# Performance work log

Measured on AMD Instinct MI355X. Metric: run time of the kernel, lower is better.

Reference implementation:

```python
import jax, jax.numpy as jnp
import numpy as np

# Model dims
B, N, D_MODEL, N_HEADS = 8, 4096, 512, 8
EXPAND = 2
D1 = (EXPAND * D_MODEL) // N_HEADS * N_HEADS      # 1024
HEAD_DIM = D1 // N_HEADS                          # 128
RANK, NK = 32, 16
GAMMA = 0.999


def setup_inputs() -> dict:
    key = jax.random.key(0)
    ks = jax.random.split(key, 24)

    def p(i, shape, std=0.02):
        return std * jax.random.normal(ks[i], shape, dtype=jnp.float32)

    def toep_params(i0):
        # SKI low-rank Toeplitz operator params: kernel values at NK inducing
        # lag positions, factorized as (h, nk, r) @ (h, r, d), plus lag-0 term.
        return (p(i0, (N_HEADS, 1, HEAD_DIM), 1.0),        # zero lag
                p(i0 + 1, (N_HEADS, NK, RANK), 0.1),       # pos lags A
                p(i0 + 2, (N_HEADS, RANK, HEAD_DIM), 0.1), # pos lags B
                p(i0 + 3, (N_HEADS, NK, RANK), 0.1),       # neg lags A
                p(i0 + 4, (N_HEADS, RANK, HEAD_DIM), 0.1)) # neg lags B

    t1 = toep_params(7)
    t2 = toep_params(12)
    return {
        'x': jax.random.normal(ks[0], (B, N, D_MODEL), dtype=jnp.float32),
        'u_w': p(1, (D1, D_MODEL)), 'u_b': p(2, (D1,)),
        'v_w': p(3, (D1, D_MODEL)), 'v_b': p(4, (D1,)),
        'o_w': p(5, (D_MODEL, D1)), 'o_b': p(6, (D_MODEL,)),
        't1_zero': t1[0], 't1_pa': t1[1], 't1_pb': t1[2], 't1_na': t1[3], 't1_nb': t1[4],
        't2_zero': t2[0], 't2_pa': t2[1], 't2_pb': t2[2], 't2_na': t2[3], 't2_nb': t2[4],
    }


def _build_kernel(zero, pos_a, pos_b, neg_a, neg_b, n):
    """Build circular-conv kernel a of shape (h, 2n, d): a[k]=t(k), a[2n-k]=t(-k)."""
    h, nk, _ = pos_a.shape
    d = pos_b.shape[-1]
    tm_pos = jnp.einsum('hkr,hrd->hkd', pos_a, pos_b)   # kernel at inducing lags
    tm_neg = jnp.einsum('hkr,hrd->hkd', neg_a, neg_b)
    lags = jnp.arange(1, n, dtype=jnp.float32)          # lags 1..n-1
    # linear interpolation from NK inducing points to n-1 lags
    pos_f = (lags - 1.0) / max(n - 2, 1) * (nk - 1)
    lo = jnp.floor(pos_f).astype(jnp.int32)
    hi = jnp.minimum(lo + 1, nk - 1)
    w = (pos_f - lo)[None, :, None]
    decay = (GAMMA ** lags)[None, :, None]              # exponential decay bias
    t_pos = ((1.0 - w) * tm_pos[:, lo] + w * tm_pos[:, hi]) * decay
    t_neg = ((1.0 - w) * tm_neg[:, lo] + w * tm_neg[:, hi]) * decay
    return jnp.concatenate(
        [zero, t_pos, jnp.zeros((h, 1, d), t_pos.dtype), jnp.flip(t_neg, axis=1)],
        axis=1)


def _toep_apply(x, zero, pos_a, pos_b, neg_a, neg_b):
    # x: (b, n, g) with g = h*d; multi-head Toeplitz mixing along axis 1 via FFT.
    b, n, g = x.shape
    h = zero.shape[0]
    d = g // h
    xh = x.reshape(b, n, h, d).transpose(0, 2, 1, 3)    # (b, h, n, d)
    a = _build_kernel(zero, pos_a, pos_b, neg_a, neg_b, n)  # (h, 2n, d)
    y = jnp.fft.irfft(
        jnp.fft.rfft(xh, 2 * n, axis=2) * jnp.fft.rfft(a, axis=1)[None],
        2 * n, axis=2)[:, :, :n]
    return y.transpose(0, 2, 1, 3).reshape(b, n, g)


def reference(x, u_w, u_b, v_w, v_b, o_w, o_b,
              t1_zero, t1_pa, t1_pb, t1_na, t1_nb,
              t2_zero, t2_pa, t2_pb, t2_na, t2_nb):
    b, n, _ = x.shape
    H = int(np.sqrt(n))
    W = n // H
    u = jax.nn.silu(x @ u_w.T + u_b)
    v = jax.nn.silu(x @ v_w.T + v_b)
    g = v.shape[-1]
    t1 = (t1_zero, t1_pa, t1_pb, t1_na, t1_nb)
    t2 = (t2_zero, t2_pa, t2_pb, t2_na, t2_nb)
    # path 1: mix along W (rows) with toep1, then along H (cols) with toep2
    o1 = _toep_apply(v.reshape(b * H, W, g), *t1)
    o1 = o1.reshape(b, H, W, g).transpose(0, 2, 1, 3).reshape(b * W, H, g)
    o1 = _toep_apply(o1, *t2)
    o1 = o1.reshape(b, W, H, g).transpose(0, 2, 1, 3).reshape(b, H * W, g)
    # path 2: mix along H with toep2, then along W with toep1
    v2 = v.reshape(b, H, W, g).transpose(0, 2, 1, 3).reshape(b * W, H, g)
    o2 = _toep_apply(v2, *t2)
    o2 = o2.reshape(b, W, H, g).transpose(0, 2, 1, 3).reshape(b * H, W, g)
    o2 = _toep_apply(o2, *t1)
    o2 = o2.reshape(b, H * W, g)
    # SiLU gate + output projection
    return (u * (o1 + o2)) @ o_w.T + o_b
```

## Files before the change

kernel.cpp:

```cpp
#include <hip/hip_runtime.h>
#include <hip/hip_bf16.h>
#include <hip/hip_fp16.h>

typedef __bf16 bf16;
typedef bf16 bf16x2 __attribute__((ext_vector_type(2)));
typedef bf16 bf16x4 __attribute__((ext_vector_type(4)));
typedef bf16 bf16x8 __attribute__((ext_vector_type(8)));
typedef float f32x2 __attribute__((ext_vector_type(2)));
typedef float f32x4 __attribute__((ext_vector_type(4)));

__device__ __forceinline__ void gload_lds16(const void* g, void* l) {
  __builtin_amdgcn_global_load_lds((__attribute__((address_space(1))) void*)g,
                                   (__attribute__((address_space(3))) void*)l,
                                   16, 0, 0);
}

__device__ __forceinline__ f32x2 fma2(f32x2 a, f32x2 b, f32x2 c) {
  return __builtin_elementwise_fma(a, b, c);
}


__global__ void cast_f32_to_bf16(const float* __restrict__ in, bf16* __restrict__ out, int n4) {
  int i = blockIdx.x * blockDim.x + threadIdx.x;
  if (i >= n4) return;
  float4 v = ((const float4*)in)[i];
  bf16x4 o = {(bf16)v.x, (bf16)v.y, (bf16)v.z, (bf16)v.w};
  ((bf16x4*)out)[i] = o;
}

__global__ void cast_w3(const float* __restrict__ uw, const float* __restrict__ vw,
                        const float* __restrict__ ow,
                        bf16* __restrict__ wuv, bf16* __restrict__ owb) {
  int t = blockIdx.x * 256 + threadIdx.x;
  int r = t >> 17;
  int i = t & 131071;
  const float* src = (r == 0) ? uw : (r == 1) ? vw : ow;
  bf16* dst = (r == 2) ? owb : (wuv + (r == 1) * 524288);
  float4 v = ((const float4*)src)[i];
  bf16x4 o = {(bf16)v.x, (bf16)v.y, (bf16)v.z, (bf16)v.w};
  ((bf16x4*)dst)[i] = o;
}

__global__ void concat_bias(const float* __restrict__ ub, const float* __restrict__ vb,
                            float* __restrict__ buv) {
  int i = blockIdx.x * blockDim.x + threadIdx.x;
  if (i < 1024) { buv[i] = ub[i]; buv[1024 + i] = vb[i]; }
}

__global__ void build_tkf(const float* __restrict__ zero, const float* __restrict__ pa,
                          const float* __restrict__ pb, const float* __restrict__ na,
                          const float* __restrict__ nb, float* __restrict__ Tkf,
                          float scale) {
  int idx = blockIdx.x * blockDim.x + threadIdx.x;
  if (idx >= 8 * 127 * 128) return;
  int d = idx & 127;
  int lagIdx = (idx >> 7) % 127;
  int h = idx / (128 * 127);
  int lag = lagIdx - 63;
  float val;
  if (lag == 0) {
    val = zero[h * 128 + d];
  } else {
    int k = lag > 0 ? lag : -lag;
    const float* A  = lag > 0 ? pa : na;
    const float* Bm = lag > 0 ? pb : nb;
    float pos_f = (float)(k - 1) * (15.0f / 62.0f);
    int lo = (int)floorf(pos_f);
    int hi = min(lo + 1, 15);
    float w = pos_f - (float)lo;
    float s = 0.f;
    for (int r = 0; r < 32; ++r) {
      float c = (1.f - w) * A[(h * 16 + lo) * 32 + r] + w * A[(h * 16 + hi) * 32 + r];
      s += c * Bm[(h * 32 + r) * 128 + d];
    }
    val = s * powf(0.999f, (float)k);
  }
  Tkf[idx] = val * scale;
}


template<int MODE>
__global__ __launch_bounds__(512, 2)
void gemm8(const bf16* __restrict__ A, const bf16* __restrict__ Bm,
           const float* __restrict__ bias,
           bf16* __restrict__ out_u, bf16* __restrict__ out_v,
           float* __restrict__ out_f, int M, int N, int K) {
  __shared__ __align__(16) char lds[131072];
  const int tid  = threadIdx.x;
  const int lane = tid & 63;
  const int l15  = lane & 15;
  const int lk16 = ((lane >> 4) & 3) << 4;
  const int w    = tid >> 6;
  const int wm   = (w >> 2) << 7;
  const int wn   = (w & 3) << 6;
  const int nbn  = N >> 8;
  const int cpx  = gridDim.x >> 3;
  const int swzb = (blockIdx.x & 7) * cpx + (blockIdx.x >> 3);
  const int br   = (swzb / nbn) << 8;
  const int bc   = (swzb % nbn) << 8;
  const int wub  = __builtin_amdgcn_readfirstlane(tid & 448);
  const int nkt  = K >> 6;

  f32x4 acc[8][4] = {};

  auto stage = [&](int kt, int b) {
    const int k0 = kt << 6;
    char* Al = lds + b * 65536;
    char* Bl = Al + 32768;
#pragma unroll
    for (int g = 0; g < 4; ++g) {
      const int flat = g * 512 + tid;
      const int row  = flat >> 3;
      const int cb   = ((flat & 7) << 4) ^ ((row & 7) << 4);
      gload_lds16((const char*)(A  + (size_t)(br + row) * K + k0) + cb,
                  Al + (g * 512 + wub) * 16);
      gload_lds16((const char*)(Bm + (size_t)(bc + row) * K + k0) + cb,
                  Bl + (g * 512 + wub) * 16);
    }
  };

  stage(0, 0);
  __syncthreads();

  for (int kt = 0; kt < nkt; ++kt) {
    const int b = kt & 1;
    const char* Ab = lds + b * 65536;
    const char* Bb = Ab + 32768;
    if (kt + 1 < nkt) stage(kt + 1, b ^ 1);
#pragma unroll
    for (int ks = 0; ks < 2; ++ks) {
      bf16x8 bfr[4];
#pragma unroll
      for (int n = 0; n < 4; ++n) {
        const int row = wn + n * 16 + l15;
        bfr[n] = *(const bf16x8*)(Bb + row * 128 + (((ks << 6) | lk16) ^ ((row & 7) << 4)));
      }
#pragma unroll
      for (int ph = 0; ph < 2; ++ph) {
        bf16x8 af[4];
#pragma unroll
        for (int mi = 0; mi < 4; ++mi) {
          const int row = wm + (ph * 4 + mi) * 16 + l15;
          af[mi] = *(const bf16x8*)(Ab + row * 128 + (((ks << 6) | lk16) ^ ((row & 7) << 4)));
        }
        __builtin_amdgcn_s_setprio(1);
#pragma unroll
        for (int mi = 0; mi < 4; ++mi)
#pragma unroll
          for (int n = 0; n < 4; ++n)
            acc[ph * 4 + mi][n] = __builtin_amdgcn_mfma_f32_16x16x32_bf16(
                af[mi], bfr[n], acc[ph * 4 + mi][n], 0, 0, 0);
        __builtin_amdgcn_s_setprio(0);
        if (ks * 2 + ph < 3) __builtin_amdgcn_s_barrier();
      }
    }
    __syncthreads();
  }

  const int lr4 = ((lane >> 4) & 3) << 2;
  if (MODE == 0) {
    const bool isU = (bc < 1024);
    bf16* outp = isU ? out_u : out_v;
    const int obc = bc & 1023;
#pragma unroll
    for (int m = 0; m < 8; ++m) {
#pragma unroll
      for (int n = 0; n < 4; ++n) {
        const int colg = bc + wn + n * 16 + l15;
        const int ocol = obc + wn + n * 16 + l15;
        const float bv = bias[colg];
#pragma unroll
        for (int r = 0; r < 4; ++r) {
          const int row = br + wm + m * 16 + lr4 + r;
          float xv = acc[m][n][r] + bv;
          float s  = xv / (1.f + __expf(-xv));
          outp[(size_t)row * 1024 + ocol] = (bf16)s;
        }
      }
    }
  } else {
#pragma unroll
    for (int m = 0; m < 8; ++m) {
#pragma unroll
      for (int n = 0; n < 4; ++n) {
        const int col = bc + wn + n * 16 + l15;
        const float bv = bias[col];
#pragma unroll
        for (int r = 0; r < 4; ++r) {
          const int row = br + wm + m * 16 + lr4 + r;
          out_f[(size_t)row * N + col] = acc[m][n][r] + bv;
        }
      }
    }
  }
}


#define VROW 130

template<int FUSE>
__global__ __launch_bounds__(256, 3)
void toep_pass(const bf16* __restrict__ in, const float* __restrict__ Tkf,
               const bf16* __restrict__ ufuse, bf16* __restrict__ out,
               int stride_j, int stride_row) {
  __shared__ float vbuf[64 * VROW];
  const int tid    = threadIdx.x;
  const int lane   = tid & 63;
  const int rowIdx = blockIdx.x >> 3;
  const int head   = blockIdx.x & 7;
  const size_t base = (size_t)(rowIdx >> 6) * 4194304
                    + (size_t)(rowIdx & 63) * stride_row + head * 128;

  const int i0 = (tid >> 6) << 4;
  const float* tg = Tkf + head * 127 * 128 + (lane << 1);

  f32x2 t[31];
#pragma unroll
  for (int s = 0; s < 31; ++s)
    t[s] = *(const f32x2*)(tg + (i0 + 48 + s) * 128);

#pragma unroll
  for (int it = 0; it < 2; ++it) {
    int c  = it * 256 + tid;
    int j  = c >> 3;
    int cg = c & 7;
    const bf16* p = in + base + (size_t)j * stride_j + cg * 16;
    bf16x8 a0 = *(const bf16x8*)p;
    bf16x8 a1 = *(const bf16x8*)(p + 8);
    f32x4 f0 = {(float)a0[0], (float)a0[1], (float)a0[2], (float)a0[3]};
    f32x4 f1 = {(float)a0[4], (float)a0[5], (float)a0[6], (float)a0[7]};
    f32x4 f2 = {(float)a1[0], (float)a1[1], (float)a1[2], (float)a1[3]};
    f32x4 f3 = {(float)a1[4], (float)a1[5], (float)a1[6], (float)a1[7]};
    float* dst = &vbuf[j * VROW + cg * 16];
    *(f32x4*)(dst)      = f0;
    *(f32x4*)(dst + 4)  = f1;
    *(f32x4*)(dst + 8)  = f2;
    *(f32x4*)(dst + 12) = f3;
  }
  __syncthreads();

  f32x2 acc[16] = {};
#pragma unroll
  for (int jb = 0; jb < 4; ++jb) {
    f32x2 p16[16];
    if (jb < 3) {
#pragma unroll
      for (int s = 0; s < 16; ++s)
        p16[s] = *(const f32x2*)(tg + (i0 - 16 * (jb + 1) + 48 + s) * 128);
    }
#pragma unroll
    for (int jj = 0; jj < 16; ++jj) {
      f32x2 v2 = *(const f32x2*)&vbuf[(jb * 16 + jj) * VROW + (lane << 1)];
#pragma unroll
      for (int ii = 0; ii < 16; ++ii)
        acc[ii] = fma2(t[ii - jj + 15], v2, acc[ii]);
    }
    if (jb < 3) {
#pragma unroll
      for (int s = 30; s >= 16; --s) t[s] = t[s - 16];
#pragma unroll
      for (int s = 0; s < 16; ++s) t[s] = p16[s];
    }
  }

  const int d0 = lane << 1;
#pragma unroll
  for (int ii = 0; ii < 16; ++ii) {
    const size_t oidx = base + (size_t)(i0 + ii) * stride_j + d0;
    float a0 = acc[ii].x, a1 = acc[ii].y;
    if (FUSE) {
      bf16x2 uu = *(const bf16x2*)(ufuse + oidx);
      a0 *= (float)uu[0];
      a1 *= (float)uu[1];
    }
    bf16x2 o2 = {(bf16)a0, (bf16)a1};
    *(bf16x2*)(out + oidx) = o2;
  }
}


extern "C" void kernel_launch(void* const* d_in, const int* in_sizes, int n_in,
                              void* d_out, int out_size, void* d_ws, size_t ws_size,
                              hipStream_t stream) {
  const float* x    = (const float*)d_in[0];
  const float* u_w  = (const float*)d_in[1];
  const float* u_b  = (const float*)d_in[2];
  const float* v_w  = (const float*)d_in[3];
  const float* v_b  = (const float*)d_in[4];
  const float* o_w  = (const float*)d_in[5];
  const float* o_b  = (const float*)d_in[6];
  const float* t1z  = (const float*)d_in[7];
  const float* t1pa = (const float*)d_in[8];
  const float* t1pb = (const float*)d_in[9];
  const float* t1na = (const float*)d_in[10];
  const float* t1nb = (const float*)d_in[11];
  const float* t2z  = (const float*)d_in[12];
  const float* t2pa = (const float*)d_in[13];
  const float* t2pb = (const float*)d_in[14];
  const float* t2na = (const float*)d_in[15];
  const float* t2nb = (const float*)d_in[16];

  char* ws = (char*)d_ws;
  size_t off = 0;
  auto alloc = [&](size_t bytes) {
    char* p = ws + off;
    off += (bytes + 255) & ~(size_t)255;
    return p;
  };
  bf16*  xb   = (bf16*)alloc(32768ull * 512 * 2);
  bf16*  wuv  = (bf16*)alloc(2048ull * 512 * 2);
  bf16*  owb  = (bf16*)alloc(512ull * 1024 * 2);
  float* buv  = (float*)alloc(2048ull * 4);
  float* Tkf1 = (float*)alloc(8ull * 127 * 128 * 4);
  float* Tkf2 = (float*)alloc(8ull * 127 * 128 * 4);
  bf16*  u    = (bf16*)alloc(32768ull * 1024 * 2);
  bf16*  v    = (bf16*)alloc(32768ull * 1024 * 2);
  bf16*  tmid = (bf16*)alloc(32768ull * 1024 * 2);
  bf16*  g    = v;

  cast_f32_to_bf16<<<16384, 256, 0, stream>>>(x, xb, 16777216 / 4);
  cast_w3<<<1536, 256, 0, stream>>>(u_w, v_w, o_w, wuv, owb);
  concat_bias<<<4, 256, 0, stream>>>(u_b, v_b, buv);
  build_tkf<<<508, 256, 0, stream>>>(t1z, t1pa, t1pb, t1na, t1nb, Tkf1, 1.0f);
  build_tkf<<<508, 256, 0, stream>>>(t2z, t2pa, t2pb, t2na, t2nb, Tkf2, 2.0f);

  gemm8<0><<<1024, 512, 0, stream>>>(xb, wuv, buv, u, v, nullptr, 32768, 2048, 512);
  toep_pass<0><<<4096, 256, 0, stream>>>(v, Tkf1, nullptr, tmid, 1024, 65536);
  toep_pass<1><<<4096, 256, 0, stream>>>(tmid, Tkf2, u, g, 65536, 1024);
  gemm8<1><<<256, 512, 0, stream>>>(g, owb, o_b, nullptr, nullptr, (float*)d_out,
                                    32768, 512, 1024);
}
```

Baseline: 303.3 us.

## Switch GEMM to triple-buffered BK=32 pipeline with vmcnt waits

The bf16 MFMA GEMM moves from a double-buffered K-tile of 64 to a triple-buffered K-tile of 32. Loads are issued two tiles ahead, and the per-tile __syncthreads is replaced by an s_waitcnt vmcnt plus a single barrier, so global-to-LDS loads overlap more with compute. This also drops the XOR swizzle on LDS rows and shrinks LDS to 96KB. The SiLU epilogue now uses a hardware reciprocal instead of a division. The risks are LDS bank conflicts from the unswizzled 64-byte rows and more barriers per unit of K.

```diff
diff --git a/kernel.cpp b/kernel.cpp
--- a/kernel.cpp
+++ b/kernel.cpp
@@ -17,6 +17,10 @@
 
 __device__ __forceinline__ f32x2 fma2(f32x2 a, f32x2 b, f32x2 c) {
   return __builtin_elementwise_fma(a, b, c);
+}
+
+__device__ __forceinline__ float silu_f(float xv) {
+  return xv * __builtin_amdgcn_rcpf(1.f + __expf(-xv));
 }
 
 
@@ -85,7 +89,7 @@
            const float* __restrict__ bias,
            bf16* __restrict__ out_u, bf16* __restrict__ out_v,
            float* __restrict__ out_f, int M, int N, int K) {
-  __shared__ __align__(16) char lds[131072];
+  __shared__ __align__(16) char lds[98304];
   const int tid  = threadIdx.x;
   const int lane = tid & 63;
   const int l15  = lane & 15;
@@ -99,19 +103,19 @@
   const int br   = (swzb / nbn) << 8;
   const int bc   = (swzb % nbn) << 8;
   const int wub  = __builtin_amdgcn_readfirstlane(tid & 448);
-  const int nkt  = K >> 6;
+  const int nkt  = K >> 5;
 
   f32x4 acc[8][4] = {};
 
   auto stage = [&](int kt, int b) {
-    const int k0 = kt << 6;
-    char* Al = lds + b * 65536;
-    char* Bl = Al + 32768;
-#pragma unroll
-    for (int g = 0; g < 4; ++g) {
+    const int k0 = kt << 5;
+    char* Al = lds + b * 32768;
+    char* Bl = Al + 16384;
+#pragma unroll
+    for (int g = 0; g < 2; ++g) {
       const int flat = g * 512 + tid;
-      const int row  = flat >> 3;
-      const int cb   = ((flat & 7) << 4) ^ ((row & 7) << 4);
+      const int row  = flat >> 2;
+      const int cb   = (flat & 3) << 4;
       gload_lds16((const char*)(A  + (size_t)(br + row) * K + k0) + cb,
                   Al + (g * 512 + wub) * 16);
       gload_lds16((const char*)(Bm + (size_t)(bc + row) * K + k0) + cb,
@@ -120,41 +124,32 @@
   };
 
   stage(0, 0);
-  __syncthreads();
-
+  stage(1, 1);
+
+  int b = 0;
   for (int kt = 0; kt < nkt; ++kt) {
-    const int b = kt & 1;
-    const char* Ab = lds + b * 65536;
-    const char* Bb = Ab + 32768;
-    if (kt + 1 < nkt) stage(kt + 1, b ^ 1);
-#pragma unroll
-    for (int ks = 0; ks < 2; ++ks) {
-      bf16x8 bfr[4];
-#pragma unroll
-      for (int n = 0; n < 4; ++n) {
-        const int row = wn + n * 16 + l15;
-        bfr[n] = *(const bf16x8*)(Bb + row * 128 + (((ks << 6) | lk16) ^ ((row & 7) << 4)));
-      }
-#pragma unroll
-      for (int ph = 0; ph < 2; ++ph) {
-        bf16x8 af[4];
-#pragma unroll
-        for (int mi = 0; mi < 4; ++mi) {
-          const int row = wm + (ph * 4 + mi) * 16 + l15;
-          af[mi] = *(const bf16x8*)(Ab + row * 128 + (((ks << 6) | lk16) ^ ((row & 7) << 4)));
-        }
-        __builtin_amdgcn_s_setprio(1);
-#pragma unroll
-        for (int mi = 0; mi < 4; ++mi)
-#pragma unroll
-          for (int n = 0; n < 4; ++n)
-            acc[ph * 4 + mi][n] = __builtin_amdgcn_mfma_f32_16x16x32_bf16(
-                af[mi], bfr[n], acc[ph * 4 + mi][n], 0, 0, 0);
-        __builtin_amdgcn_s_setprio(0);
-        if (ks * 2 + ph < 3) __builtin_amdgcn_s_barrier();
-      }
-    }
-    __syncthreads();
+    if (kt + 1 < nkt) asm volatile("s_waitcnt vmcnt(4)" ::: "memory");
+    else              asm volatile("s_waitcnt vmcnt(0)" ::: "memory");
+    __builtin_amdgcn_s_barrier();
+    __builtin_amdgcn_sched_barrier(0);
+    if (kt + 2 < nkt) stage(kt + 2, b == 0 ? 2 : b - 1);
+
+    const char* Ab = lds + b * 32768;
+    const char* Bb = Ab + 16384;
+    bf16x8 bfr[4];
+#pragma unroll
+    for (int n = 0; n < 4; ++n)
+      bfr[n] = *(const bf16x8*)(Bb + (wn + n * 16 + l15) * 64 + lk16);
+    __builtin_amdgcn_s_setprio(1);
+#pragma unroll
+    for (int m = 0; m < 8; ++m) {
+      bf16x8 af = *(const bf16x8*)(Ab + (wm + m * 16 + l15) * 64 + lk16);
+#pragma unroll
+      for (int n = 0; n < 4; ++n)
+        acc[m][n] = __builtin_amdgcn_mfma_f32_16x16x32_bf16(af, bfr[n], acc[m][n], 0, 0, 0);
+    }
+    __builtin_amdgcn_s_setprio(0);
+    b = (b == 2) ? 0 : b + 1;
   }
 
   const int lr4 = ((lane >> 4) & 3) << 2;
@@ -172,9 +167,7 @@
 #pragma unroll
         for (int r = 0; r < 4; ++r) {
           const int row = br + wm + m * 16 + lr4 + r;
-          float xv = acc[m][n][r] + bv;
-          float s  = xv / (1.f + __expf(-xv));
-          outp[(size_t)row * 1024 + ocol] = (bf16)s;
+          outp[(size_t)row * 1024 + ocol] = (bf16)silu_f(acc[m][n][r] + bv);
         }
       }
     }
```

Measured after the change: 292.9 us. 1.04x faster.
